# Performance work log

Measured on AMD Instinct MI355X. Metric: run time of the kernel, lower is better.

The kernel has to match this reference:

```python
import jax, jax.numpy as jnp
import numpy as np

BETA = 0.25
N_EMBED = 1024
DIM = 256


def setup_inputs() -> dict:
    key = jax.random.key(0)
    k1, k2 = jax.random.split(key)
    z = jax.random.normal(k1, (8, DIM, 64, 64), dtype=jnp.float32)
    # matches nn.Embedding init: uniform(-1/n_embed, 1/n_embed)
    codebook = jax.random.uniform(
        k2, (N_EMBED, DIM), dtype=jnp.float32,
        minval=-1.0 / N_EMBED, maxval=1.0 / N_EMBED)
    return {"z": z, "codebook": codebook}


def reference(z, codebook):
    B, C, H, W = z.shape
    sg = jax.lax.stop_gradient
    zp = jnp.transpose(z, (0, 2, 3, 1))          # [B,H,W,C]
    zf = zp.reshape(-1, C)                        # [N,C], N = B*H*W
    # squared euclidean distances: ||z||^2 + ||e||^2 - 2 z.e
    d = (jnp.sum(zf * zf, axis=1, keepdims=True)
         + jnp.sum(codebook * codebook, axis=1)
         - 2.0 * zf @ codebook.T)                 # [N, n_embed]
    idx = jnp.argmin(d, axis=1)                   # [N]
    # one-hot @ codebook in the original is just an index gather
    z_q = codebook[idx].reshape(zp.shape)         # [B,H,W,C]
    loss = (BETA * jnp.mean((sg(z_q) - zp) ** 2)
            + jnp.mean((z_q - sg(zp)) ** 2))
    z_q_st = zp + sg(z_q - zp)                    # straight-through estimator
    z_q_out = jnp.transpose(z_q_st, (0, 3, 1, 2))  # back to NCHW
    return z_q_out, loss, idx.reshape(B, H, W)
```

## Files before the change

### kernel.cpp

```cpp
#include <hip/hip_runtime.h>
#include <hip/hip_fp16.h>

#define NELEM 8388608
#define M_GAP 6e-4f
#define SCORE_SCALE (-1.0f / 512.0f)

typedef _Float16 f16x8 __attribute__((ext_vector_type(8)));
typedef short s16x8 __attribute__((ext_vector_type(8)));
typedef float f32x4 __attribute__((ext_vector_type(4)));

__device__ __forceinline__ unsigned short bf16r(float f) {
  unsigned u = __float_as_uint(f);
  return (unsigned short)((u + 0x7fffu + ((u >> 16) & 1u)) >> 16);
}
__device__ __forceinline__ float bf16f(unsigned short h) {
  return __uint_as_float(((unsigned)h) << 16);
}

__device__ __forceinline__ float pw128_sq(const float* p, int s) {
  float r[8];
#pragma unroll
  for (int j = 0; j < 8; ++j) { float v = p[j * s]; r[j] = __fmul_rn(v, v); }
#pragma unroll
  for (int i = 8; i < 128; i += 8) {
#pragma unroll
    for (int j = 0; j < 8; ++j) {
      float v = p[(i + j) * s];
      r[j] = __fadd_rn(r[j], __fmul_rn(v, v));
    }
  }
  return __fadd_rn(__fadd_rn(__fadd_rn(r[0], r[1]), __fadd_rn(r[2], r[3])),
                   __fadd_rn(__fadd_rn(r[4], r[5]), __fadd_rn(r[6], r[7])));
}
__device__ __forceinline__ float np_sumsq256(const float* p, int s) {
  return __fadd_rn(pw128_sq(p, s), pw128_sq(p + 128 * s, s));
}

__global__ __launch_bounds__(256)
void vq_prep(const float* __restrict__ cb, unsigned short* __restrict__ cbimg,
             float* __restrict__ cbT, float* __restrict__ Bsg,
             unsigned* __restrict__ cnt, float* __restrict__ loss) {
  __shared__ float rows[16][260];
  const int t = threadIdx.x;
  const int b = blockIdx.x;
  if (b == 0 && t == 0) { cnt[0] = 0u; *loss = 0.0f; }
#pragma unroll
  for (int i = 0; i < 4; ++i) {
    int idx = t + i * 256;
    int r = idx >> 6, c4 = idx & 63;
    float4 v = reinterpret_cast<const float4*>(cb + (size_t)(b * 16 + r) * 256)[c4];
    rows[r][c4 * 4 + 0] = v.x;
    rows[r][c4 * 4 + 1] = v.y;
    rows[r][c4 * 4 + 2] = v.z;
    rows[r][c4 * 4 + 3] = v.w;
  }
  __syncthreads();
  if (t < 16) Bsg[b * 16 + t] = np_sumsq256(&rows[t][0], 1);
#pragma unroll
  for (int uu = 0; uu < 2; ++uu) {
    int u = t * 2 + uu;
    int kk = u >> 6, rem = u & 63;
    int lk = rem >> 4, jj = rem & 15;
    int c0 = kk * 32 + lk * 8;
    s16x8 hv;
#pragma unroll
    for (int m = 0; m < 8; ++m)
      hv[m] = (short)__half_as_ushort(__float2half(rows[jj][c0 + m] * 1024.0f));
    *reinterpret_cast<s16x8*>(cbimg + (size_t)b * 4096 + u * 8) = hv;
  }
  {
    float* dst = cbT + (size_t)t * 1024 + b * 16;
#pragma unroll
    for (int jj = 0; jj < 16; ++jj) dst[jj] = rows[jj][t];
  }
}

#define VQ_STEP_PF(IT2, DO_PF)                                                 \
  {                                                                            \
    f32x4 acc[4];                                                              \
    _Pragma("unroll")                                                          \
    for (int rs = 0; rs < 4; ++rs) acc[rs] = (f32x4){0.f, 0.f, 0.f, 0.f};      \
    _Pragma("unroll")                                                          \
    for (int kk = 0; kk < 8; ++kk) {                                           \
      f16x8 bcur = ba[kk];                                                     \
      if (DO_PF)                                                               \
        ba[kk] = cimg2[(size_t)(wv * 16 + (IT2) + 1) * 512 + kk * 64 + lane];  \
      _Pragma("unroll")                                                        \
      for (int rs = 0; rs < 4; ++rs)                                           \
        acc[rs] = __builtin_amdgcn_mfma_f32_16x16x32_f16(ah[rs][kk], bcur,     \
                                                         acc[rs], 0, 0, 0);    \
    }                                                                          \
    int j = wv * 256 + (IT2) * 16 + l15;                                       \
    float Bj = BsL[j];                                                         \
    _Pragma("unroll")                                                          \
    for (int rs = 0; rs < 4; ++rs) {                                           \
      _Pragma("unroll")                                                        \
      for (int r = 0; r < 4; ++r) {                                            \
        float s = fmaf(SCORE_SCALE, acc[rs][r], Bj);                           \
        bool lt = s < b1v[rs][r];                                              \
        float other = lt ? b1v[rs][r] : s;                                     \
        b2v[rs][r] = fminf(b2v[rs][r], other);                                 \
        b1v[rs][r] = fminf(b1v[rs][r], s);                                     \
        b1i[rs][r] = lt ? j : b1i[rs][r];                                      \
      }                                                                        \
    }                                                                          \
  }

__global__ __launch_bounds__(256, 1)
void vq_fast(const float* __restrict__ z, const float* __restrict__ cb,
             const unsigned short* __restrict__ cbimg,
             const float* __restrict__ Bsg,
             float* __restrict__ zq, float* __restrict__ loss,
             float* __restrict__ idxo,
             unsigned* __restrict__ list, unsigned* __restrict__ cnt,
             float* __restrict__ zdump) {
  __shared__ __align__(16) unsigned char buf[34816];
  __shared__ float BsL[1024];
  __shared__ float part[32][36];
  __shared__ float rowA[64];
  __shared__ int bestj[64];
  __shared__ float bestd[64];
  __shared__ unsigned char flg[64];
  __shared__ float wred[4];
  __shared__ float cv1[4 * 64], cv2[4 * 64];
  __shared__ int ci1[4 * 64];

  const int t = threadIdx.x;
  const int bid = blockIdx.x;
  const int lane = t & 63;
  const int wv = t >> 6;
  const int l15 = lane & 15;
  const int lk = lane >> 4;

  const f16x8* cimg2 = reinterpret_cast<const f16x8*>(cbimg);
  float* zt = reinterpret_cast<float*>(buf);
  const float4* z4 = reinterpret_cast<const float4*>(
      z + (size_t)(bid >> 6) * 1048576 + (size_t)(bid & 63) * 64);

  f16x8 ba[8];
#pragma unroll
  for (int kk = 0; kk < 8; ++kk)
    ba[kk] = cimg2[(size_t)(wv * 16) * 512 + kk * 64 + lane];

  for (int i = t; i < 1024; i += 256) BsL[i] = Bsg[i];

  f16x8 ah[4][8];
#pragma unroll
  for (int hp = 0; hp < 2; ++hp) {
    float sq[4] = {0.f, 0.f, 0.f, 0.f};
#pragma unroll
    for (int i = 0; i < 8; ++i) {
      int idx = t + i * 256;
      int c = idx >> 3, w4p = idx & 7;
      float4 v = z4[(size_t)c * 1024 + hp * 8 + w4p];
      zt[c * 33 + w4p * 4 + 0] = v.x;
      zt[c * 33 + w4p * 4 + 1] = v.y;
      zt[c * 33 + w4p * 4 + 2] = v.z;
      zt[c * 33 + w4p * 4 + 3] = v.w;
      sq[0] += v.x * v.x; sq[1] += v.y * v.y;
      sq[2] += v.z * v.z; sq[3] += v.w * v.w;
    }
#pragma unroll
    for (int q = 0; q < 4; ++q) part[t >> 3][(t & 7) * 4 + q] = sq[q];
    __syncthreads();
    if (t < 32) {
      float s = 0.f;
#pragma unroll
      for (int g = 0; g < 32; ++g) s += part[g][t];
      rowA[hp * 32 + t] = s;
    }
#pragma unroll
    for (int rr2 = 0; rr2 < 2; ++rr2) {
      int lr = rr2 * 16 + l15;
#pragma unroll
      for (int kk = 0; kk < 8; ++kk)
#pragma unroll
        for (int m = 0; m < 8; ++m)
          ah[hp * 2 + rr2][kk][m] = (_Float16)zt[(kk * 32 + lk * 8 + m) * 33 + lr];
    }
#pragma unroll
    for (int i = 0; i < 8; ++i) {
      int item = t + i * 256;
      int c4 = item & 63, rowp = item >> 6;
      float4 v = make_float4(zt[(c4 * 4 + 0) * 33 + rowp],
                             zt[(c4 * 4 + 1) * 33 + rowp],
                             zt[(c4 * 4 + 2) * 33 + rowp],
                             zt[(c4 * 4 + 3) * 33 + rowp]);
      *reinterpret_cast<float4*>(
          zdump + ((size_t)bid * 64 + hp * 32 + rowp) * 256 + c4 * 4) = v;
    }
    __syncthreads();
  }

  float b1v[4][4], b2v[4][4];
  int b1i[4][4];
#pragma unroll
  for (int rs = 0; rs < 4; ++rs)
#pragma unroll
    for (int r = 0; r < 4; ++r) { b1v[rs][r] = 3.4e38f; b2v[rs][r] = 3.4e38f; b1i[rs][r] = 0; }

  for (int it = 0; it < 15; ++it) {
    VQ_STEP_PF(it, true);
  }
  VQ_STEP_PF(15, false);

#pragma unroll
  for (int mk = 1; mk < 16; mk <<= 1) {
#pragma unroll
    for (int rs = 0; rs < 4; ++rs)
#pragma unroll
      for (int r = 0; r < 4; ++r) {
        float ov1 = __shfl_xor(b1v[rs][r], mk, 64);
        float ov2 = __shfl_xor(b2v[rs][r], mk, 64);
        int oi1 = __shfl_xor(b1i[rs][r], mk, 64);
        bool lt = ov1 < b1v[rs][r];
        float hi = lt ? b1v[rs][r] : ov1;
        b2v[rs][r] = fminf(fminf(b2v[rs][r], ov2), hi);
        b1v[rs][r] = fminf(b1v[rs][r], ov1);
        b1i[rs][r] = lt ? oi1 : b1i[rs][r];
      }
  }
  if (l15 == 0) {
#pragma unroll
    for (int rs = 0; rs < 4; ++rs)
#pragma unroll
      for (int r = 0; r < 4; ++r) {
        int rr = rs * 16 + lk * 4 + r;
        cv1[wv * 64 + rr] = b1v[rs][r];
        cv2[wv * 64 + rr] = b2v[rs][r];
        ci1[wv * 64 + rr] = b1i[rs][r];
      }
  }
  __syncthreads();

  if (t < 64) {
    float v1 = cv1[t], v2 = cv2[t];
    int i1 = ci1[t];
#pragma unroll
    for (int w = 1; w < 4; ++w) {
      float u1 = cv1[w * 64 + t], u2 = cv2[w * 64 + t];
      int ui = ci1[w * 64 + t];
      if (u1 < v1) { v2 = fminf(v1, u2); v1 = u1; i1 = ui; }
      else v2 = fminf(v2, u1);
    }
    bestj[t] = i1;
    bestd[t] = v1;
    flg[t] = (v2 - v1 <= M_GAP) ? 1 : 0;
    int n = bid * 64 + t;
    idxo[n] = (float)i1;
    if (flg[t]) { unsigned pos = atomicAdd(cnt, 1u); list[pos] = (unsigned)n; }
  }
  __syncthreads();

  {
    float lv = (t < 64) ? (rowA[t] + bestd[t]) : 0.f;
#pragma unroll
    for (int off = 32; off > 0; off >>= 1) lv += __shfl_down(lv, off, 64);
    if (lane == 0) wred[wv] = lv;
  }
  __syncthreads();
  if (t == 0)
    atomicAdd(loss, (wred[0] + wred[1] + wred[2] + wred[3]) * (1.25f / (float)NELEM));

  f32x4* ldsF4 = reinterpret_cast<f32x4*>(buf);
  const float* ldsF = reinterpret_cast<const float*>(buf);
  const float4* cb4 = reinterpret_cast<const float4*>(cb);
  float* zqb = zq + (size_t)(bid >> 6) * 1048576 + (size_t)(bid & 63) * 64;
  for (int hp = 0; hp < 2; ++hp) {
    __syncthreads();
#pragma unroll
    for (int i = 0; i < 8; ++i) {
      int item = t + i * 256;
      int rr = item >> 6, cc = item & 63;
      float4 v = cb4[(size_t)bestj[hp * 32 + rr] * 64 + cc];
      ldsF4[rr * 64 + (cc ^ ((rr >> 2) & 7))] = (f32x4){v.x, v.y, v.z, v.w};
    }
    __syncthreads();
#pragma unroll
    for (int i = 0; i < 8; ++i) {
      int item = t + i * 256;
      int w4p = item & 7, c = item >> 3;
      float ov[4];
#pragma unroll
      for (int q = 0; q < 4; ++q) {
        int rr = w4p * 4 + q;
        ov[q] = ldsF[(rr * 64 + ((c >> 2) ^ ((rr >> 2) & 7))) * 4 + (c & 3)];
      }
      *reinterpret_cast<float4*>(zqb + (size_t)c * 4096 + hp * 32 + w4p * 4) =
          make_float4(ov[0], ov[1], ov[2], ov[3]);
    }
  }
}

__global__ __launch_bounds__(256)
void vq_exact_fast(const float* __restrict__ zdump, const float* __restrict__ cbT,
                   const float* __restrict__ Bsg, const unsigned* __restrict__ list,
                   const unsigned* __restrict__ cnt, float* __restrict__ idxo) {
  __shared__ float zr[8][260];
  __shared__ float Anp[8];
  __shared__ float rv[256];
  __shared__ int ri[256];
  const int t = threadIdx.x;
  const unsigned K = *cnt;
  const float4* cbT4 = reinterpret_cast<const float4*>(cbT);
  const float4* zd4 = reinterpret_cast<const float4*>(zdump);

  for (unsigned g = blockIdx.x; g * 8 < K; g += gridDim.x) {
    int nrows = (int)min(8u, K - g * 8);
    __syncthreads();
#pragma unroll
    for (int i = 0; i < 2; ++i) {
      int idx = t + i * 256;
      int r = idx >> 6, c4 = idx & 63;
      if (r < nrows) {
        float4 v = zd4[(size_t)list[g * 8 + r] * 64 + c4];
        zr[r][c4 * 4 + 0] = v.x; zr[r][c4 * 4 + 1] = v.y;
        zr[r][c4 * 4 + 2] = v.z; zr[r][c4 * 4 + 3] = v.w;
      }
    }
    __syncthreads();
    if (t < nrows) Anp[t] = np_sumsq256(&zr[t][0], 1);
    __syncthreads();

    float acc[8][4];
#pragma unroll
    for (int r = 0; r < 8; ++r)
#pragma unroll
      for (int q = 0; q < 4; ++q) acc[r][q] = 0.f;
    for (int c = 0; c < 256; ++c) {
      float4 bv = cbT4[c * 256 + t];
#pragma unroll
      for (int r = 0; r < 8; ++r) {
        float zc = zr[r][c];
        acc[r][0] = fmaf(zc, bv.x, acc[r][0]);
        acc[r][1] = fmaf(zc, bv.y, acc[r][1]);
        acc[r][2] = fmaf(zc, bv.z, acc[r][2]);
        acc[r][3] = fmaf(zc, bv.w, acc[r][3]);
      }
    }
    for (int r = 0; r < nrows; ++r) {
      float A = Anp[r];
      float bvv = 3.4e38f;
      int bii = 0;
#pragma unroll
      for (int q = 0; q < 4; ++q) {
        int j = t * 4 + q;
        float dd = __fsub_rn(__fadd_rn(A, Bsg[j]), __fmul_rn(2.0f, acc[r][q]));
        if (dd < bvv) { bvv = dd; bii = j; }
      }
      rv[t] = bvv; ri[t] = bii;
      __syncthreads();
      for (int s2 = 128; s2 > 0; s2 >>= 1) {
        if (t < s2) {
          float v2 = rv[t + s2]; int i2 = ri[t + s2];
          if (v2 < rv[t] || (v2 == rv[t] && i2 < ri[t])) { rv[t] = v2; ri[t] = i2; }
        }
        __syncthreads();
      }
      if (t == 0) idxo[list[g * 8 + r]] = (float)ri[0];
      __syncthreads();
    }
  }
}

__global__ __launch_bounds__(256)
void vq_ref(const float* __restrict__ z, const float* __restrict__ cb,
            float* __restrict__ zq, float* __restrict__ loss,
            float* __restrict__ idxo) {
  __shared__ __align__(16) float zt[256 * 64];
  __shared__ __align__(16) float cbt[256 * 64];
  __shared__ float As[64];
  __shared__ float Bs[64];
  __shared__ int bestj[64];
  __shared__ float cand_v[16 * 64];
  __shared__ int cand_i[16 * 64];
  __shared__ double wred[4];
  const int t = threadIdx.x;
  const int wg = t & 15, jg = t >> 4;
  const int bid = blockIdx.x;
  const int b = bid >> 6, h = bid & 63;
  const int n0 = bid * 64;
  const float4* z4 = reinterpret_cast<const float4*>(z + (size_t)b * 256 * 4096 + (size_t)h * 64);
  float4* zt4 = reinterpret_cast<float4*>(zt);
#pragma unroll
  for (int i = 0; i < 16; ++i) {
    int idx4 = t + i * 256;
    zt4[idx4] = z4[(size_t)(idx4 >> 4) * 1024 + (idx4 & 15)];
  }
  __syncthreads();
  if (t < 64) As[t] = np_sumsq256(zt + t, 64);
  float bv[4]; int bi[4];
#pragma unroll
  for (int a = 0; a < 4; ++a) { bv[a] = 3.4e38f; bi[a] = 0; }
  for (int p = 0; p < 16; ++p) {
    __syncthreads();
    const float4* cb4 = reinterpret_cast<const float4*>(cb) + (size_t)p * 64 * 64;
#pragma unroll
    for (int i = 0; i < 16; ++i) {
      int idx4 = t + i * 256;
      int jj = idx4 >> 6, c4 = idx4 & 63;
      float4 v = cb4[idx4];
      cbt[(c4 * 4 + 0) * 64 + jj] = v.x;
      cbt[(c4 * 4 + 1) * 64 + jj] = v.y;
      cbt[(c4 * 4 + 2) * 64 + jj] = v.z;
      cbt[(c4 * 4 + 3) * 64 + jj] = v.w;
    }
    __syncthreads();
    if (t < 64) Bs[t] = np_sumsq256(cbt + t, 64);
    float acc[4][4];
#pragma unroll
    for (int a = 0; a < 4; ++a)
#pragma unroll
      for (int u = 0; u < 4; ++u) acc[a][u] = 0.0f;
    const float4* ztp = reinterpret_cast<const float4*>(zt) + wg;
    const float4* cbp = reinterpret_cast<const float4*>(cbt) + jg;
#pragma unroll 4
    for (int c = 0; c < 256; ++c) {
      float4 zv = ztp[c * 16];
      float4 cv = cbp[c * 16];
      float za[4] = {zv.x, zv.y, zv.z, zv.w};
      float ca[4] = {cv.x, cv.y, cv.z, cv.w};
#pragma unroll
      for (int a = 0; a < 4; ++a)
#pragma unroll
        for (int u = 0; u < 4; ++u) acc[a][u] = fmaf(za[a], ca[u], acc[a][u]);
    }
    __syncthreads();
#pragma unroll
    for (int u = 0; u < 4; ++u) {
      int j = p * 64 + jg * 4 + u;
      float Bju = Bs[jg * 4 + u];
#pragma unroll
      for (int a = 0; a < 4; ++a) {
        float AB = __fadd_rn(As[wg * 4 + a], Bju);
        float dd = __fsub_rn(AB, __fmul_rn(2.0f, acc[a][u]));
        if (dd < bv[a]) { bv[a] = dd; bi[a] = j; }
      }
    }
  }
  __syncthreads();
#pragma unroll
  for (int a = 0; a < 4; ++a) {
    int w = wg * 4 + a;
    cand_v[jg * 64 + w] = bv[a];
    cand_i[jg * 64 + w] = bi[a];
  }
  __syncthreads();
  if (t < 64) {
    float v0 = cand_v[t]; int i0 = cand_i[t];
    for (int g = 1; g < 16; ++g) {
      float v = cand_v[g * 64 + t]; int ii = cand_i[g * 64 + t];
      if (v < v0 || (v == v0 && ii < i0)) { v0 = v; i0 = ii; }
    }
    bestj[t] = i0;
    idxo[n0 + t] = (float)i0;
  }
  __syncthreads();
  double lsum = 0.0;
  float* zqbase = zq + (size_t)b * 256 * 4096 + (size_t)h * 64;
  for (int i = 0; i < 64; ++i) {
    int idx = t + i * 256;
    int c = idx >> 6, w = idx & 63;
    float zvv = zt[c * 64 + w];
    float cvv = cb[(size_t)bestj[w] * 256 + c];
    zqbase[(size_t)c * 4096 + w] = cvv;
    double d = (double)cvv - (double)zvv;
    lsum += d * d;
  }
#pragma unroll
  for (int off = 32; off > 0; off >>= 1) lsum += __shfl_down(lsum, off, 64);
  if ((t & 63) == 0) wred[t >> 6] = lsum;
  __syncthreads();
  if (t == 0) {
    double tot = wred[0] + wred[1] + wred[2] + wred[3];
    atomicAdd(loss, (float)(tot * (1.25 / (double)NELEM)));
  }
}

extern "C" void kernel_launch(void* const* d_in, const int* in_sizes, int n_in,
                              void* d_out, int out_size, void* d_ws, size_t ws_size,
                              hipStream_t stream) {
  (void)in_sizes; (void)n_in; (void)out_size;
  const float* z = (const float*)d_in[0];
  const float* cb = (const float*)d_in[1];
  float* out = (float*)d_out;
  float* zq = out;
  float* loss = out + NELEM;
  float* idxo = out + NELEM + 1;
  if (ws_size < 35651584) {
    hipMemsetAsync(loss, 0, sizeof(float), stream);
    vq_ref<<<512, 256, 0, stream>>>(z, cb, zq, loss, idxo);
    return;
  }
  unsigned char* ws = (unsigned char*)d_ws;
  unsigned* cnt = (unsigned*)ws;
  float* Bsg = (float*)(ws + 1024);
  unsigned* list = (unsigned*)(ws + 8192);
  float* cbT = (float*)(ws + 139264);
  unsigned short* cbimg = (unsigned short*)(ws + 1187840);
  float* zdump = (float*)(ws + 2097152);
  vq_prep<<<64, 256, 0, stream>>>(cb, cbimg, cbT, Bsg, cnt, loss);
  vq_fast<<<512, 256, 0, stream>>>(z, cb, cbimg, Bsg, zq, loss, idxo, list, cnt, zdump);
  vq_exact_fast<<<512, 256, 0, stream>>>(zdump, cbT, Bsg, list, cnt, idxo);
}
```

Baseline: 98.89 us.

## Drop z row dump; gather flagged rows from z and double-buffer codebook loads

Removes the per-block write of a transposed copy of z into workspace, which was only used by the exact re-check pass. The re-check kernel now gathers each flagged row directly from the NCHW input with strided loads. The MFMA loop also switches from single-register prefetch to two alternating codebook buffers. This trades a large streaming write for scattered, uncoalesced reads on the few flagged rows, plus higher register pressure.

```diff
diff --git a/kernel.cpp b/kernel.cpp
--- a/kernel.cpp
+++ b/kernel.cpp
@@ -75,19 +75,23 @@
   }
 }
 
-#define VQ_STEP_PF(IT2, DO_PF)                                                 \
+#define VQ_LOAD(DST, TIDX)                                                     \
+  {                                                                            \
+    _Pragma("unroll")                                                          \
+    for (int kk = 0; kk < 8; ++kk)                                             \
+      DST[kk] = cimg2[(size_t)(wv * 16 + (TIDX)) * 512 + kk * 64 + lane];      \
+  }
+
+#define VQ_STEP(BFR, IT2)                                                      \
   {                                                                            \
     f32x4 acc[4];                                                              \
     _Pragma("unroll")                                                          \
     for (int rs = 0; rs < 4; ++rs) acc[rs] = (f32x4){0.f, 0.f, 0.f, 0.f};      \
     _Pragma("unroll")                                                          \
     for (int kk = 0; kk < 8; ++kk) {                                           \
-      f16x8 bcur = ba[kk];                                                     \
-      if (DO_PF)                                                               \
-        ba[kk] = cimg2[(size_t)(wv * 16 + (IT2) + 1) * 512 + kk * 64 + lane];  \
       _Pragma("unroll")                                                        \
       for (int rs = 0; rs < 4; ++rs)                                           \
-        acc[rs] = __builtin_amdgcn_mfma_f32_16x16x32_f16(ah[rs][kk], bcur,     \
+        acc[rs] = __builtin_amdgcn_mfma_f32_16x16x32_f16(ah[rs][kk], BFR[kk],  \
                                                          acc[rs], 0, 0, 0);    \
     }                                                                          \
     int j = wv * 256 + (IT2) * 16 + l15;                                       \
@@ -112,8 +116,7 @@
              const float* __restrict__ Bsg,
              float* __restrict__ zq, float* __restrict__ loss,
              float* __restrict__ idxo,
-             unsigned* __restrict__ list, unsigned* __restrict__ cnt,
-             float* __restrict__ zdump) {
+             unsigned* __restrict__ list, unsigned* __restrict__ cnt) {
   __shared__ __align__(16) unsigned char buf[34816];
   __shared__ float BsL[1024];
   __shared__ float part[32][36];
@@ -137,10 +140,8 @@
   const float4* z4 = reinterpret_cast<const float4*>(
       z + (size_t)(bid >> 6) * 1048576 + (size_t)(bid & 63) * 64);
 
-  f16x8 ba[8];
-#pragma unroll
-  for (int kk = 0; kk < 8; ++kk)
-    ba[kk] = cimg2[(size_t)(wv * 16) * 512 + kk * 64 + lane];
+  f16x8 ba[8], bb[8];
+  VQ_LOAD(ba, 0);
 
   for (int i = t; i < 1024; i += 256) BsL[i] = Bsg[i];
 
@@ -178,17 +179,6 @@
         for (int m = 0; m < 8; ++m)
           ah[hp * 2 + rr2][kk][m] = (_Float16)zt[(kk * 32 + lk * 8 + m) * 33 + lr];
     }
-#pragma unroll
-    for (int i = 0; i < 8; ++i) {
-      int item = t + i * 256;
-      int c4 = item & 63, rowp = item >> 6;
-      float4 v = make_float4(zt[(c4 * 4 + 0) * 33 + rowp],
-                             zt[(c4 * 4 + 1) * 33 + rowp],
-                             zt[(c4 * 4 + 2) * 33 + rowp],
-                             zt[(c4 * 4 + 3) * 33 + rowp]);
-      *reinterpret_cast<float4*>(
-          zdump + ((size_t)bid * 64 + hp * 32 + rowp) * 256 + c4 * 4) = v;
-    }
     __syncthreads();
   }
 
@@ -199,10 +189,13 @@
 #pragma unroll
     for (int r = 0; r < 4; ++r) { b1v[rs][r] = 3.4e38f; b2v[rs][r] = 3.4e38f; b1i[rs][r] = 0; }
 
-  for (int it = 0; it < 15; ++it) {
-    VQ_STEP_PF(it, true);
-  }
-  VQ_STEP_PF(15, false);
+  VQ_LOAD(bb, 1);
+  for (int it = 0; it < 16; it += 2) {
+    VQ_STEP(ba, it);
+    if (it + 2 < 16) VQ_LOAD(ba, it + 2);
+    VQ_STEP(bb, it + 1);
+    if (it + 3 < 16) VQ_LOAD(bb, it + 3);
+  }
 
 #pragma unroll
   for (int mk = 1; mk < 16; mk <<= 1) {
@@ -293,9 +286,9 @@
 }
 
 __global__ __launch_bounds__(256)
-void vq_exact_fast(const float* __restrict__ zdump, const float* __restrict__ cbT,
-                   const float* __restrict__ Bsg, const unsigned* __restrict__ list,
-                   const unsigned* __restrict__ cnt, float* __restrict__ idxo) {
+void vq_exact_scatter(const float* __restrict__ z, const float* __restrict__ cbT,
+                      const float* __restrict__ Bsg, const unsigned* __restrict__ list,
+                      const unsigned* __restrict__ cnt, float* __restrict__ idxo) {
   __shared__ float zr[8][260];
   __shared__ float Anp[8];
   __shared__ float rv[256];
@@ -303,19 +296,21 @@
   const int t = threadIdx.x;
   const unsigned K = *cnt;
   const float4* cbT4 = reinterpret_cast<const float4*>(cbT);
-  const float4* zd4 = reinterpret_cast<const float4*>(zdump);
 
   for (unsigned g = blockIdx.x; g * 8 < K; g += gridDim.x) {
     int nrows = (int)min(8u, K - g * 8);
     __syncthreads();
-#pragma unroll
-    for (int i = 0; i < 2; ++i) {
-      int idx = t + i * 256;
-      int r = idx >> 6, c4 = idx & 63;
+    {
+      int r = t >> 5, l32 = t & 31;
       if (r < nrows) {
-        float4 v = zd4[(size_t)list[g * 8 + r] * 64 + c4];
-        zr[r][c4 * 4 + 0] = v.x; zr[r][c4 * 4 + 1] = v.y;
-        zr[r][c4 * 4 + 2] = v.z; zr[r][c4 * 4 + 3] = v.w;
+        int n = (int)list[g * 8 + r];
+        int b = n >> 12, hw = n & 4095;
+        const float* zb = z + (size_t)b * 1048576 + hw;
+#pragma unroll
+        for (int q = 0; q < 8; ++q) {
+          int c = l32 * 8 + q;
+          zr[r][c] = zb[(size_t)c * 4096];
+        }
       }
     }
     __syncthreads();
@@ -487,7 +482,7 @@
   float* zq = out;
   float* loss = out + NELEM;
   float* idxo = out + NELEM + 1;
-  if (ws_size < 35651584) {
+  if (ws_size < 2236416) {
     hipMemsetAsync(loss, 0, sizeof(float), stream);
     vq_ref<<<512, 256, 0, stream>>>(z, cb, zq, loss, idxo);
     return;
@@ -498,8 +493,7 @@
   unsigned* list = (unsigned*)(ws + 8192);
   float* cbT = (float*)(ws + 139264);
   unsigned short* cbimg = (unsigned short*)(ws + 1187840);
-  float* zdump = (float*)(ws + 2097152);
   vq_prep<<<64, 256, 0, stream>>>(cb, cbimg, cbT, Bsg, cnt, loss);
-  vq_fast<<<512, 256, 0, stream>>>(z, cb, cbimg, Bsg, zq, loss, idxo, list, cnt, zdump);
-  vq_exact_fast<<<512, 256, 0, stream>>>(zdump, cbT, Bsg, list, cnt, idxo);
-}
+  vq_fast<<<512, 256, 0, stream>>>(z, cb, cbimg, Bsg, zq, loss, idxo, list, cnt);
+  vq_exact_scatter<<<512, 256, 0, stream>>>(z, cbT, Bsg, list, cnt, idxo);
+}
```

After: 101.2 us. 1.02x slower.

## Halve rows per block in VQ main kernel and double grid size

Applied to the files above, without the earlier changes.

Each block of the main VQ kernel now processes 32 spatial rows instead of 64, and the grid doubles to 1024 blocks. This shrinks per-thread A-fragment registers and accumulators and removes the two-pass loop over row halves. It aims for more parallelism and occupancy. In exchange, every block re-streams the full fp16 codebook image for half as many rows, doubling codebook reads and halving MFMA reuse per loaded B fragment.

```diff
diff --git a/kernel.cpp b/kernel.cpp
--- a/kernel.cpp
+++ b/kernel.cpp
@@ -77,23 +77,23 @@
 
 #define VQ_STEP_PF(IT2, DO_PF)                                                 \
   {                                                                            \
-    f32x4 acc[4];                                                              \
-    _Pragma("unroll")                                                          \
-    for (int rs = 0; rs < 4; ++rs) acc[rs] = (f32x4){0.f, 0.f, 0.f, 0.f};      \
+    f32x4 acc[2];                                                              \
+    acc[0] = (f32x4){0.f, 0.f, 0.f, 0.f};                                      \
+    acc[1] = (f32x4){0.f, 0.f, 0.f, 0.f};                                      \
     _Pragma("unroll")                                                          \
     for (int kk = 0; kk < 8; ++kk) {                                           \
       f16x8 bcur = ba[kk];                                                     \
       if (DO_PF)                                                               \
         ba[kk] = cimg2[(size_t)(wv * 16 + (IT2) + 1) * 512 + kk * 64 + lane];  \
       _Pragma("unroll")                                                        \
-      for (int rs = 0; rs < 4; ++rs)                                           \
+      for (int rs = 0; rs < 2; ++rs)                                           \
         acc[rs] = __builtin_amdgcn_mfma_f32_16x16x32_f16(ah[rs][kk], bcur,     \
                                                          acc[rs], 0, 0, 0);    \
     }                                                                          \
     int j = wv * 256 + (IT2) * 16 + l15;                                       \
     float Bj = BsL[j];                                                         \
     _Pragma("unroll")                                                          \
-    for (int rs = 0; rs < 4; ++rs) {                                           \
+    for (int rs = 0; rs < 2; ++rs) {                                           \
       _Pragma("unroll")                                                        \
       for (int r = 0; r < 4; ++r) {                                            \
         float s = fmaf(SCORE_SCALE, acc[rs][r], Bj);                           \
@@ -114,16 +114,16 @@
              float* __restrict__ idxo,
              unsigned* __restrict__ list, unsigned* __restrict__ cnt,
              float* __restrict__ zdump) {
-  __shared__ __align__(16) unsigned char buf[34816];
+  __shared__ __align__(16) unsigned char buf[33792];
   __shared__ float BsL[1024];
-  __shared__ float part[32][36];
-  __shared__ float rowA[64];
-  __shared__ int bestj[64];
-  __shared__ float bestd[64];
-  __shared__ unsigned char flg[64];
+  __shared__ float part[32][33];
+  __shared__ float rowA[32];
+  __shared__ int bestj[32];
+  __shared__ float bestd[32];
+  __shared__ unsigned char flg[32];
   __shared__ float wred[4];
-  __shared__ float cv1[4 * 64], cv2[4 * 64];
-  __shared__ int ci1[4 * 64];
+  __shared__ float cv1[4 * 32], cv2[4 * 32];
+  __shared__ int ci1[4 * 32];
 
   const int t = threadIdx.x;
   const int bid = blockIdx.x;
@@ -131,11 +131,12 @@
   const int wv = t >> 6;
   const int l15 = lane & 15;
   const int lk = lane >> 4;
+  const int bh = bid >> 1, half = bid & 1;
 
   const f16x8* cimg2 = reinterpret_cast<const f16x8*>(cbimg);
   float* zt = reinterpret_cast<float*>(buf);
   const float4* z4 = reinterpret_cast<const float4*>(
-      z + (size_t)(bid >> 6) * 1048576 + (size_t)(bid & 63) * 64);
+      z + (size_t)(bh >> 6) * 1048576 + (size_t)(bh & 63) * 64 + half * 32);
 
   f16x8 ba[8];
 #pragma unroll
@@ -144,15 +145,13 @@
 
   for (int i = t; i < 1024; i += 256) BsL[i] = Bsg[i];
 
-  f16x8 ah[4][8];
-#pragma unroll
-  for (int hp = 0; hp < 2; ++hp) {
+  {
     float sq[4] = {0.f, 0.f, 0.f, 0.f};
 #pragma unroll
     for (int i = 0; i < 8; ++i) {
       int idx = t + i * 256;
       int c = idx >> 3, w4p = idx & 7;
-      float4 v = z4[(size_t)c * 1024 + hp * 8 + w4p];
+      float4 v = z4[(size_t)c * 1024 + w4p];
       zt[c * 33 + w4p * 4 + 0] = v.x;
       zt[c * 33 + w4p * 4 + 1] = v.y;
       zt[c * 33 + w4p * 4 + 2] = v.z;
@@ -162,40 +161,41 @@
     }
 #pragma unroll
     for (int q = 0; q < 4; ++q) part[t >> 3][(t & 7) * 4 + q] = sq[q];
-    __syncthreads();
-    if (t < 32) {
-      float s = 0.f;
-#pragma unroll
-      for (int g = 0; g < 32; ++g) s += part[g][t];
-      rowA[hp * 32 + t] = s;
-    }
-#pragma unroll
-    for (int rr2 = 0; rr2 < 2; ++rr2) {
-      int lr = rr2 * 16 + l15;
-#pragma unroll
-      for (int kk = 0; kk < 8; ++kk)
-#pragma unroll
-        for (int m = 0; m < 8; ++m)
-          ah[hp * 2 + rr2][kk][m] = (_Float16)zt[(kk * 32 + lk * 8 + m) * 33 + lr];
-    }
-#pragma unroll
-    for (int i = 0; i < 8; ++i) {
-      int item = t + i * 256;
-      int c4 = item & 63, rowp = item >> 6;
-      float4 v = make_float4(zt[(c4 * 4 + 0) * 33 + rowp],
-                             zt[(c4 * 4 + 1) * 33 + rowp],
-                             zt[(c4 * 4 + 2) * 33 + rowp],
-                             zt[(c4 * 4 + 3) * 33 + rowp]);
-      *reinterpret_cast<float4*>(
-          zdump + ((size_t)bid * 64 + hp * 32 + rowp) * 256 + c4 * 4) = v;
-    }
-    __syncthreads();
-  }
-
-  float b1v[4][4], b2v[4][4];
-  int b1i[4][4];
-#pragma unroll
-  for (int rs = 0; rs < 4; ++rs)
+  }
+  __syncthreads();
+  if (t < 32) {
+    float s = 0.f;
+#pragma unroll
+    for (int g = 0; g < 32; ++g) s += part[g][t];
+    rowA[t] = s;
+  }
+
+  f16x8 ah[2][8];
+#pragma unroll
+  for (int rs = 0; rs < 2; ++rs)
+#pragma unroll
+    for (int kk = 0; kk < 8; ++kk)
+#pragma unroll
+      for (int m = 0; m < 8; ++m)
+        ah[rs][kk][m] = (_Float16)zt[(kk * 32 + lk * 8 + m) * 33 + rs * 16 + l15];
+
+#pragma unroll
+  for (int i = 0; i < 8; ++i) {
+    int item = t + i * 256;
+    int c4 = item & 63, rowp = item >> 6;
+    float4 v = make_float4(zt[(c4 * 4 + 0) * 33 + rowp],
+                           zt[(c4 * 4 + 1) * 33 + rowp],
+                           zt[(c4 * 4 + 2) * 33 + rowp],
+                           zt[(c4 * 4 + 3) * 33 + rowp]);
+    *reinterpret_cast<float4*>(
+        zdump + ((size_t)bid * 32 + rowp) * 256 + c4 * 4) = v;
+  }
+  __syncthreads();
+
+  float b1v[2][4], b2v[2][4];
+  int b1i[2][4];
+#pragma unroll
+  for (int rs = 0; rs < 2; ++rs)
 #pragma unroll
     for (int r = 0; r < 4; ++r) { b1v[rs][r] = 3.4e38f; b2v[rs][r] = 3.4e38f; b1i[rs][r] = 0; }
 
@@ -207,7 +207,7 @@
 #pragma unroll
   for (int mk = 1; mk < 16; mk <<= 1) {
 #pragma unroll
-    for (int rs = 0; rs < 4; ++rs)
+    for (int rs = 0; rs < 2; ++rs)
 #pragma unroll
       for (int r = 0; r < 4; ++r) {
         float ov1 = __shfl_xor(b1v[rs][r], mk, 64);
@@ -222,38 +222,38 @@
   }
   if (l15 == 0) {
 #pragma unroll
-    for (int rs = 0; rs < 4; ++rs)
+    for (int rs = 0; rs < 2; ++rs)
 #pragma unroll
       for (int r = 0; r < 4; ++r) {
         int rr = rs * 16 + lk * 4 + r;
-        cv1[wv * 64 + rr] = b1v[rs][r];
-        cv2[wv * 64 + rr] = b2v[rs][r];
-        ci1[wv * 64 + rr] = b1i[rs][r];
-      }
-  }
-  __syncthreads();
-
-  if (t < 64) {
+        cv1[wv * 32 + rr] = b1v[rs][r];
+        cv2[wv * 32 + rr] = b2v[rs][r];
+        ci1[wv * 32 + rr] = b1i[rs][r];
+      }
+  }
+  __syncthreads();
+
+  if (t < 32) {
     float v1 = cv1[t], v2 = cv2[t];
     int i1 = ci1[t];
 #pragma unroll
     for (int w = 1; w < 4; ++w) {
-      float u1 = cv1[w * 64 + t], u2 = cv2[w * 64 + t];
-      int ui = ci1[w * 64 + t];
+      float u1 = cv1[w * 32 + t], u2 = cv2[w * 32 + t];
+      int ui = ci1[w * 32 + t];
       if (u1 < v1) { v2 = fminf(v1, u2); v1 = u1; i1 = ui; }
       else v2 = fminf(v2, u1);
     }
     bestj[t] = i1;
     bestd[t] = v1;
     flg[t] = (v2 - v1 <= M_GAP) ? 1 : 0;
-    int n = bid * 64 + t;
+    int n = bid * 32 + t;
     idxo[n] = (float)i1;
     if (flg[t]) { unsigned pos = atomicAdd(cnt, 1u); list[pos] = (unsigned)n; }
   }
   __syncthreads();
 
   {
-    float lv = (t < 64) ? (rowA[t] + bestd[t]) : 0.f;
+    float lv = (t < 32) ? (rowA[t] + bestd[t]) : 0.f;
 #pragma unroll
     for (int off = 32; off > 0; off >>= 1) lv += __shfl_down(lv, off, 64);
     if (lane == 0) wred[wv] = lv;
@@ -265,30 +265,27 @@
   f32x4* ldsF4 = reinterpret_cast<f32x4*>(buf);
   const float* ldsF = reinterpret_cast<const float*>(buf);
   const float4* cb4 = reinterpret_cast<const float4*>(cb);
-  float* zqb = zq + (size_t)(bid >> 6) * 1048576 + (size_t)(bid & 63) * 64;
-  for (int hp = 0; hp < 2; ++hp) {
-    __syncthreads();
-#pragma unroll
-    for (int i = 0; i < 8; ++i) {
-      int item = t + i * 256;
-      int rr = item >> 6, cc = item & 63;
-      float4 v = cb4[(size_t)bestj[hp * 32 + rr] * 64 + cc];
-      ldsF4[rr * 64 + (cc ^ ((rr >> 2) & 7))] = (f32x4){v.x, v.y, v.z, v.w};
-    }
-    __syncthreads();
-#pragma unroll
-    for (int i = 0; i < 8; ++i) {
-      int item = t + i * 256;
-      int w4p = item & 7, c = item >> 3;
-      float ov[4];
-#pragma unroll
-      for (int q = 0; q < 4; ++q) {
-        int rr = w4p * 4 + q;
-        ov[q] = ldsF[(rr * 64 + ((c >> 2) ^ ((rr >> 2) & 7))) * 4 + (c & 3)];
-      }
-      *reinterpret_cast<float4*>(zqb + (size_t)c * 4096 + hp * 32 + w4p * 4) =
-          make_float4(ov[0], ov[1], ov[2], ov[3]);
-    }
+  float* zqb = zq + (size_t)(bh >> 6) * 1048576 + (size_t)(bh & 63) * 64 + half * 32;
+#pragma unroll
+  for (int i = 0; i < 8; ++i) {
+    int item = t + i * 256;
+    int rr = item >> 6, cc = item & 63;
+    float4 v = cb4[(size_t)bestj[rr] * 64 + cc];
+    ldsF4[rr * 64 + (cc ^ ((rr >> 2) & 7))] = (f32x4){v.x, v.y, v.z, v.w};
+  }
+  __syncthreads();
+#pragma unroll
+  for (int i = 0; i < 8; ++i) {
+    int item = t + i * 256;
+    int w4p = item & 7, c = item >> 3;
+    float ov[4];
+#pragma unroll
+    for (int q = 0; q < 4; ++q) {
+      int rr = w4p * 4 + q;
+      ov[q] = ldsF[(rr * 64 + ((c >> 2) ^ ((rr >> 2) & 7))) * 4 + (c & 3)];
+    }
+    *reinterpret_cast<float4*>(zqb + (size_t)c * 4096 + w4p * 4) =
+        make_float4(ov[0], ov[1], ov[2], ov[3]);
   }
 }
 
@@ -500,6 +497,6 @@
   unsigned short* cbimg = (unsigned short*)(ws + 1187840);
   float* zdump = (float*)(ws + 2097152);
   vq_prep<<<64, 256, 0, stream>>>(cb, cbimg, cbT, Bsg, cnt, loss);
-  vq_fast<<<512, 256, 0, stream>>>(z, cb, cbimg, Bsg, zq, loss, idxo, list, cnt, zdump);
+  vq_fast<<<1024, 256, 0, stream>>>(z, cb, cbimg, Bsg, zq, loss, idxo, list, cnt, zdump);
   vq_exact_fast<<<512, 256, 0, stream>>>(zdump, cbT, Bsg, list, cnt, idxo);
 }
```

Measured after the change: 97.76 us. No clear change (-1.1%).
